# Performance work log

Hardware: AMD Instinct MI355X
Metric: run time of the kernel (lower is better)

The kernel has to match this reference:

```python
import jax, jax.numpy as jnp
import numpy as np

DMODEL = 1024

def setup_inputs() -> dict:
    key = jax.random.key(0)
    ks = jax.random.split(key, 7)
    scale = 1.0 / np.sqrt(DMODEL)
    x = jax.random.normal(ks[0], (4, 2048, DMODEL), dtype=jnp.float32)
    Wq = jax.random.normal(ks[1], (DMODEL, DMODEL), dtype=jnp.float32) * scale
    bq = jnp.zeros((DMODEL,), dtype=jnp.float32)
    Wk = jax.random.normal(ks[2], (DMODEL, DMODEL), dtype=jnp.float32) * scale
    bk = jnp.zeros((DMODEL,), dtype=jnp.float32)
    Wv = jax.random.normal(ks[3], (DMODEL, DMODEL), dtype=jnp.float32) * scale
    bv = jnp.zeros((DMODEL,), dtype=jnp.float32)
    return {"x": x, "Wq": Wq, "bq": bq, "Wk": Wk, "bk": bk, "Wv": Wv, "bv": bv}

def reference(x, Wq, bq, Wk, bk, Wv, bv):
    # QKV projections: [b, s, d]
    q = jnp.einsum('bsd,de->bse', x, Wq) + bq
    k = jnp.einsum('bsd,de->bse', x, Wk) + bk
    v = jnp.einsum('bsd,de->bse', x, Wv) + bv
    # scaled dot-product attention, full [b, s, s] score matrix (as in source)
    scores = jnp.einsum('bqd,bkd->bqk', q, k) / jnp.sqrt(jnp.asarray(q.shape[-1], q.dtype))
    weights = jax.nn.softmax(scores, axis=-1)
    return jnp.einsum('bqk,bkd->bqd', weights, v)
```

## Files before the change

kernel.cpp:

```cpp
#include <hip/hip_runtime.h>

typedef unsigned short u16;
typedef __attribute__((ext_vector_type(8))) short short8;
typedef __attribute__((ext_vector_type(4))) short short4v;
typedef __attribute__((ext_vector_type(4))) float f32x4;


__device__ __forceinline__ u16 f2bf(float f) {
  union { float f; unsigned u; } c; c.f = f;
  unsigned u = c.u;
  unsigned r = u + 0x7fffu + ((u >> 16) & 1u);
  return (u16)(r >> 16);
}

__device__ __forceinline__ float bf2f(u16 b) {
  union { unsigned u; float f; } c; c.u = ((unsigned)b) << 16;
  return c.f;
}

__device__ __forceinline__ void load_lds16(const void* g, void* l) {
  __builtin_amdgcn_global_load_lds(
      (__attribute__((address_space(1))) void*)(__UINTPTR_TYPE__)(g),
      (__attribute__((address_space(3))) void*)(l),
      16, 0, 0);
}

template <int N> __device__ __forceinline__ void vm_wait() {
  if constexpr (N == 0) asm volatile("s_waitcnt vmcnt(0)");
  else if constexpr (N == 3) asm volatile("s_waitcnt vmcnt(3)");
  else if constexpr (N == 4) asm volatile("s_waitcnt vmcnt(4)");
}

template <int BM, int MODE>
__global__ __launch_bounds__(512)
void gemm256(const u16* __restrict__ A, const u16* __restrict__ Bt,
             void* __restrict__ C0, void* __restrict__ C1,
             const float* __restrict__ b0, const float* __restrict__ b1,
             const float* __restrict__ b2,
             int K, int lda, int ldb, int ldc, float scale,
             long zsA, long zsB, long zsC)
{
  constexpr int MREP = BM / 32;
  constexpr int LA   = BM / 128;
  constexpr int BOFF = BM * 64;
  constexpr int LDSE = BM * 64 + 16384;
  __shared__ __align__(16) u16 lds[2][LDSE];

  A  += (long)blockIdx.z * zsA;
  Bt += (long)blockIdx.z * zsB;

  int bxi, byi;
  if (MODE == 0 || MODE == 3) {
    const int gw   = gridDim.x;
    const int nwg  = gw * gridDim.y;
    const int orig = blockIdx.x + gw * blockIdx.y;
    const int s    = (orig & 7) * (nwg >> 3) + (orig >> 3);
    bxi = s % gw; byi = s / gw;
  } else {
    bxi = blockIdx.x; byi = blockIdx.y;
  }

  const int t    = threadIdx.x;
  const int lane = t & 63;
  const int wave = t >> 6;
  const int wr   = wave >> 2;
  const int wc   = wave & 3;
  const long brow = (long)byi * BM;
  const long bcol = (long)bxi * 256;

  f32x4 acc[MREP][4];
#pragma unroll
  for (int m = 0; m < MREP; ++m)
#pragma unroll
    for (int n = 0; n < 4; ++n)
#pragma unroll
      for (int j = 0; j < 4; ++j) acc[m][n][j] = 0.f;

  const int frA  = wr * (BM / 2) + (lane & 15);
  const int kAsw = (((lane >> 4) ^ ((frA >> 1) & 3)) * 8);
  const int frB  = wc * 64 + (lane & 15);
  const int kBsw = (((lane >> 4) ^ ((frB >> 1) & 3)) * 8);

  const int sr  = t >> 2;
  const int ssl = ((t & 3) ^ ((sr >> 1) & 3)) * 8;
  const u16* gA = A  + (size_t)(brow + sr) * lda + ssl;
  const u16* gB = Bt + (size_t)(bcol + sr) * ldb + ssl;
  const int NT = K >> 6;

#define STAGE_A(nb, kt1, ks) do {                                   \
    u16* d = &lds[(nb)][(ks) * (BM * 32) + t * 8];                  \
    const u16* g = gA + (size_t)(kt1) * 64 + (ks) * 32;             \
    load_lds16(g, d);                                               \
    if (LA == 2) load_lds16(g + (size_t)128 * lda, d + 4096);       \
  } while (0)

#define STAGE_B(nb, kt1, ks) do {                                   \
    u16* d = &lds[(nb)][BOFF + (ks) * 8192 + t * 8];                \
    const u16* g = gB + (size_t)(kt1) * 64 + (ks) * 32;             \
    load_lds16(g, d);                                               \
    load_lds16(g + (size_t)128 * ldb, d + 4096);                    \
  } while (0)

#define PHASE2(ks, STG, VM) {                                                    \
    _Pragma("unroll")                                                            \
    for (int i = 0; i < MREP; ++i)                                               \
      af[i] = *(const short8*)&bufA[(ks) * (BM * 32) +                           \
                 (size_t)(frA + i * 16) * 32 + kAsw];                            \
    _Pragma("unroll")                                                            \
    for (int n = 0; n < 4; ++n)                                                  \
      bf[n] = *(const short8*)&bufB[(ks) * 8192 +                                \
                 (size_t)(frB + n * 16) * 32 + kBsw];                            \
    STG;                                                                         \
    __builtin_amdgcn_s_barrier();                                                \
    asm volatile("s_waitcnt lgkmcnt(0)");                                        \
    __builtin_amdgcn_sched_barrier(0);                                           \
    __builtin_amdgcn_s_setprio(1);                                               \
    _Pragma("unroll")                                                            \
    for (int i = 0; i < MREP; ++i)                                               \
      _Pragma("unroll")                                                          \
      for (int n = 0; n < 4; ++n)                                                \
        acc[i][n] = __builtin_amdgcn_mfma_f32_16x16x32_bf16(                     \
            af[i], bf[n], acc[i][n], 0, 0, 0);                                   \
    __builtin_amdgcn_s_setprio(0);                                               \
    VM;                                                                          \
    __builtin_amdgcn_s_barrier();                                                \
  }

  STAGE_A(0, 0, 0); STAGE_B(0, 0, 0); STAGE_A(0, 0, 1); STAGE_B(0, 0, 1);
  vm_wait<0>();
  __builtin_amdgcn_s_barrier();

  short8 af[MREP], bf[4];
  for (int kt = 0; kt < NT - 1; ++kt) {
    const u16* bufA = &lds[kt & 1][0];
    const u16* bufB = bufA + BOFF;
    const int nb = (kt + 1) & 1;
    PHASE2(0, { STAGE_A(nb, kt + 1, 0); STAGE_B(nb, kt + 1, 0); }, vm_wait<LA + 2>())
    PHASE2(1, { STAGE_A(nb, kt + 1, 1); STAGE_B(nb, kt + 1, 1); }, vm_wait<LA + 2>())
  }
  {
    const u16* bufA = &lds[(NT - 1) & 1][0];
    const u16* bufB = bufA + BOFF;
    PHASE2(0, (void)0, vm_wait<0>())
    PHASE2(1, (void)0, (void)0)
  }
#undef PHASE2
#undef STAGE_A
#undef STAGE_B

  const int dcol = lane & 15;
  const int dr4  = (lane >> 4) * 4;
  if (MODE == 0) {
    const int which = (int)(bcol >> 10);
    const float sc = which ? 1.0f : scale;
    const float* bb = which ? b1 : b0;
    u16* dst = (u16*)C0 + (long)which * (8192L * 1024);
#pragma unroll
    for (int m = 0; m < MREP; ++m) {
#pragma unroll
      for (int n = 0; n < 4; ++n) {
        const long cp   = (bcol - ((long)which << 10)) + wc * 64 + n * 16 + dcol;
        const long row0 = brow + wr * (BM / 2) + m * 16 + dr4;
        const float bias = bb[cp];
#pragma unroll
        for (int j = 0; j < 4; ++j)
          dst[(row0 + j) * 1024 + cp] = f2bf((acc[m][n][j] + bias) * sc);
      }
    }
  } else if (MODE == 3) {
    constexpr int SMSK = BM / 4 - 1;
    u16* sm = (u16*)lds;
#pragma unroll
    for (int m = 0; m < MREP; ++m) {
#pragma unroll
      for (int n = 0; n < 4; ++n) {
        const int cpl = wc * 64 + n * 16 + dcol;
        const int r0l = wr * (BM / 2) + m * 16 + dr4;
        const float bias = b2[bcol + cpl];
        short4v w;
#pragma unroll
        for (int j = 0; j < 4; ++j) w[j] = (short)f2bf(acc[m][n][j] + bias);
        *(short4v*)&sm[cpl * BM + (((r0l >> 2) ^ (cpl & SMSK)) << 2)] = w;
      }
    }
    __syncthreads();
    u16* dst = (u16*)C1;
#pragma unroll
    for (int it = 0; it < BM / 16; ++it) {
      const int idx = it * 512 + t;
      const int i  = idx / (BM / 8);
      const int ch = idx & (BM / 8 - 1);
      const short4v lo = *(const short4v*)&sm[i * BM + ((((ch * 2)    ) ^ (i & SMSK)) << 2)];
      const short4v hi = *(const short4v*)&sm[i * BM + ((((ch * 2) + 1) ^ (i & SMSK)) << 2)];
      short8 o;
      o[0] = lo[0]; o[1] = lo[1]; o[2] = lo[2]; o[3] = lo[3];
      o[4] = hi[0]; o[5] = hi[1]; o[6] = hi[2]; o[7] = hi[3];
      *(short8*)&dst[(bcol + i) * 8192 + brow + ch * 8] = o;
    }
  } else {
#pragma unroll
    for (int m = 0; m < MREP; ++m) {
#pragma unroll
      for (int n = 0; n < 4; ++n) {
        const long col  = bcol + wc * 64 + n * 16 + dcol;
        const long row0 = brow + wr * (BM / 2) + m * 16 + dr4;
        if (MODE == 1) {
#pragma unroll
          for (int j = 0; j < 4; ++j)
            ((u16*)C0)[(long)blockIdx.z * zsC + (row0 + j) * ldc + col] =
                f2bf(acc[m][n][j] * scale);
        } else {
#pragma unroll
          for (int j = 0; j < 4; ++j)
            ((float*)C0)[(long)blockIdx.z * zsC + (row0 + j) * ldc + col] =
                acc[m][n][j];
        }
      }
    }
  }
}

__global__ __launch_bounds__(256)
void cvt_bf16(const float* __restrict__ in, u16* __restrict__ out, int n4)
{
  int i = blockIdx.x * 256 + threadIdx.x;
  const int stride = gridDim.x * 256;
  for (; i < n4; i += stride) {
    const float4 f = ((const float4*)in)[i];
    ushort4 u;
    u.x = f2bf(f.x); u.y = f2bf(f.y); u.z = f2bf(f.z); u.w = f2bf(f.w);
    ((ushort4*)out)[i] = u;
  }
}

__global__ __launch_bounds__(256)
void wtrans(const float* __restrict__ W, u16* __restrict__ Wt)
{
  __shared__ u16 tile[32][33];
  const int tx = threadIdx.x;
  const int ty = threadIdx.y;
  const int bx = blockIdx.x * 32;
  const int by = blockIdx.y * 32;
#pragma unroll
  for (int i = 0; i < 4; ++i)
    tile[ty + i * 8][tx] = f2bf(W[(size_t)(by + ty + i * 8) * 1024 + bx + tx]);
  __syncthreads();
#pragma unroll
  for (int i = 0; i < 4; ++i)
    Wt[(size_t)(bx + ty + i * 8) * 1024 + by + tx] = tile[tx][ty + i * 8];
}

__global__ __launch_bounds__(256)
void softmax_rows_bf16(u16* __restrict__ S)
{
  u16* s = S + (size_t)blockIdx.x * 2048;
  const int t = threadIdx.x;

  const short8 r = ((const short8*)s)[t];
  float v[8];
#pragma unroll
  for (int i = 0; i < 8; ++i) v[i] = bf2f((u16)r[i]);

  float m = -1e30f;
#pragma unroll
  for (int i = 0; i < 8; ++i) m = fmaxf(m, v[i]);
#pragma unroll
  for (int o = 32; o; o >>= 1) m = fmaxf(m, __shfl_xor(m, o));
  __shared__ float redm[4], reds[4];
  if ((t & 63) == 0) redm[t >> 6] = m;
  __syncthreads();
  m = fmaxf(fmaxf(redm[0], redm[1]), fmaxf(redm[2], redm[3]));

  float sum = 0.f;
#pragma unroll
  for (int i = 0; i < 8; ++i) { v[i] = __expf(v[i] - m); sum += v[i]; }
#pragma unroll
  for (int o = 32; o; o >>= 1) sum += __shfl_xor(sum, o);
  if ((t & 63) == 0) reds[t >> 6] = sum;
  __syncthreads();
  const float inv = 1.f / (reds[0] + reds[1] + reds[2] + reds[3]);

  short8 w;
#pragma unroll
  for (int i = 0; i < 8; ++i) w[i] = (short)f2bf(v[i] * inv);
  ((short8*)s)[t] = w;
}

extern "C" void kernel_launch(void* const* d_in, const int* in_sizes, int n_in,
                              void* d_out, int out_size, void* d_ws, size_t ws_size,
                              hipStream_t stream)
{
  const float* x  = (const float*)d_in[0];
  const float* Wq = (const float*)d_in[1];
  const float* bq = (const float*)d_in[2];
  const float* Wk = (const float*)d_in[3];
  const float* bk = (const float*)d_in[4];
  const float* Wv = (const float*)d_in[5];
  const float* bv = (const float*)d_in[6];
  float* out = (float*)d_out;
  char* ws = (char*)d_ws;

  const size_t MB = (size_t)1 << 20;
  const float qscale = 0.03125f;
  const long  SO = 2048L * 1024;

  u16* Qb   = (u16*)(ws);
  u16* Kb   = (u16*)(ws + 16 * MB);
  u16* Vt   = (u16*)(ws + 32 * MB);
  u16* Sc   = (u16*)(ws + 48 * MB);
  u16* xb   = (u16*)(ws + 48 * MB);
  u16* Wcat = (u16*)(ws + 80 * MB);

  cvt_bf16<<<2048, 256, 0, stream>>>(x, xb, (4 * 2048 * 1024) / 4);
  dim3 tb(32, 8), tg(32, 32);
  wtrans<<<tg, tb, 0, stream>>>(Wq, Wcat);
  wtrans<<<tg, tb, 0, stream>>>(Wk, Wcat + 1024 * 1024);
  wtrans<<<tg, tb, 0, stream>>>(Wv, Wcat + 2 * 1024 * 1024);

  gemm256<256, 0><<<dim3(8, 32), 512, 0, stream>>>(
      xb, Wcat, Qb, nullptr, bq, bk, nullptr,
      1024, 1024, 1024, 1024, qscale, 0, 0, 0);

  gemm256<128, 3><<<dim3(4, 64), 512, 0, stream>>>(
      xb, Wcat + 2 * 1024 * 1024, nullptr, Vt, nullptr, nullptr, bv,
      1024, 1024, 1024, 1024, 1.0f, 0, 0, 0);

  gemm256<256, 1><<<dim3(8, 8, 4), 512, 0, stream>>>(
      Qb, Kb, Sc, nullptr, nullptr, nullptr, nullptr,
      1024, 1024, 1024, 2048, 1.0f, SO, SO, 2048L * 2048);

  softmax_rows_bf16<<<4 * 2048, 256, 0, stream>>>(Sc);

  gemm256<128, 2><<<dim3(4, 16, 4), 512, 0, stream>>>(
      Sc, Vt, out, nullptr, nullptr, nullptr, nullptr,
      2048, 2048, 8192, 1024, 1.0f, 2048L * 2048, 2048, SO);
}
```

Measured before the change: 175.7 us.

## Fuse softmax into the PV GEMM via a per-row log-sum-exp prologue

Removes the standalone row-softmax kernel. The PV GEMM gains a new mode with a prologue that computes each row's log-sum-exp over the full bf16 score row. It then exponentiates A fragments in registers (exp(s - L)) before each MFMA step. This saves a full read and write pass over the score matrix, but it recomputes exps redundantly in every column block and adds VALU work to the GEMM main loop. It also drops max-subtraction, so large scores could overflow. The block-index swizzle is also applied to every GEMM mode now, not just modes 0 and 3.

```diff
diff --git a/kernel.cpp b/kernel.cpp
--- a/kernel.cpp
+++ b/kernel.cpp
@@ -45,20 +45,18 @@
   constexpr int BOFF = BM * 64;
   constexpr int LDSE = BM * 64 + 16384;
   __shared__ __align__(16) u16 lds[2][LDSE];
+  __shared__ float Lrow[(MODE == 4) ? 128 : 1];
+  __shared__ float psum[(MODE == 4) ? 128 : 1][4];
 
   A  += (long)blockIdx.z * zsA;
   Bt += (long)blockIdx.z * zsB;
 
-  int bxi, byi;
-  if (MODE == 0 || MODE == 3) {
-    const int gw   = gridDim.x;
-    const int nwg  = gw * gridDim.y;
-    const int orig = blockIdx.x + gw * blockIdx.y;
-    const int s    = (orig & 7) * (nwg >> 3) + (orig >> 3);
-    bxi = s % gw; byi = s / gw;
-  } else {
-    bxi = blockIdx.x; byi = blockIdx.y;
-  }
+  const int gw   = gridDim.x;
+  const int nwg  = gw * gridDim.y;
+  const int orig = blockIdx.x + gw * blockIdx.y;
+  const int sswz = (orig & 7) * (nwg >> 3) + (orig >> 3);
+  const int bxi  = sswz % gw;
+  const int byi  = sswz / gw;
 
   const int t    = threadIdx.x;
   const int lane = t & 63;
@@ -80,6 +78,27 @@
   const int kAsw = (((lane >> 4) ^ ((frA >> 1) & 3)) * 8);
   const int frB  = wc * 64 + (lane & 15);
   const int kBsw = (((lane >> 4) ^ ((frB >> 1) & 3)) * 8);
+
+  float Lm[MREP];
+  if constexpr (MODE == 4) {
+    const int r = t >> 2;
+    const int q = t & 3;
+    const u16* p = A + (size_t)(brow + r) * lda + q * 8;
+    float ps = 0.f;
+#pragma unroll 8
+    for (int i = 0; i < 64; ++i) {
+      const short8 v = *(const short8*)(p + i * 32);
+#pragma unroll
+      for (int e = 0; e < 8; ++e) ps += __expf(bf2f((u16)v[e]));
+    }
+    psum[r][q] = ps;
+    __syncthreads();
+    if (t < 128)
+      Lrow[t] = __logf(psum[t][0] + psum[t][1] + psum[t][2] + psum[t][3]);
+    __syncthreads();
+#pragma unroll
+    for (int i = 0; i < MREP; ++i) Lm[i] = Lrow[frA + i * 16];
+  }
 
   const int sr  = t >> 2;
   const int ssl = ((t & 3) ^ ((sr >> 1) & 3)) * 8;
@@ -114,6 +133,16 @@
     __builtin_amdgcn_s_barrier();                                                \
     asm volatile("s_waitcnt lgkmcnt(0)");                                        \
     __builtin_amdgcn_sched_barrier(0);                                           \
+    if constexpr (MODE == 4) {                                                   \
+      _Pragma("unroll")                                                          \
+      for (int i = 0; i < MREP; ++i) {                                           \
+        short8 a = af[i];                                                        \
+        _Pragma("unroll")                                                        \
+        for (int e = 0; e < 8; ++e)                                              \
+          a[e] = (short)f2bf(__expf(bf2f((u16)a[e]) - Lm[i]));                   \
+        af[i] = a;                                                               \
+      }                                                                          \
+    }                                                                            \
     __builtin_amdgcn_s_setprio(1);                                               \
     _Pragma("unroll")                                                            \
     for (int i = 0; i < MREP; ++i)                                               \
@@ -248,42 +277,6 @@
 #pragma unroll
   for (int i = 0; i < 4; ++i)
     Wt[(size_t)(bx + ty + i * 8) * 1024 + by + tx] = tile[tx][ty + i * 8];
-}
-
-__global__ __launch_bounds__(256)
-void softmax_rows_bf16(u16* __restrict__ S)
-{
-  u16* s = S + (size_t)blockIdx.x * 2048;
-  const int t = threadIdx.x;
-
-  const short8 r = ((const short8*)s)[t];
-  float v[8];
-#pragma unroll
-  for (int i = 0; i < 8; ++i) v[i] = bf2f((u16)r[i]);
-
-  float m = -1e30f;
-#pragma unroll
-  for (int i = 0; i < 8; ++i) m = fmaxf(m, v[i]);
-#pragma unroll
-  for (int o = 32; o; o >>= 1) m = fmaxf(m, __shfl_xor(m, o));
-  __shared__ float redm[4], reds[4];
-  if ((t & 63) == 0) redm[t >> 6] = m;
-  __syncthreads();
-  m = fmaxf(fmaxf(redm[0], redm[1]), fmaxf(redm[2], redm[3]));
-
-  float sum = 0.f;
-#pragma unroll
-  for (int i = 0; i < 8; ++i) { v[i] = __expf(v[i] - m); sum += v[i]; }
-#pragma unroll
-  for (int o = 32; o; o >>= 1) sum += __shfl_xor(sum, o);
-  if ((t & 63) == 0) reds[t >> 6] = sum;
-  __syncthreads();
-  const float inv = 1.f / (reds[0] + reds[1] + reds[2] + reds[3]);
-
-  short8 w;
-#pragma unroll
-  for (int i = 0; i < 8; ++i) w[i] = (short)f2bf(v[i] * inv);
-  ((short8*)s)[t] = w;
 }
 
 extern "C" void kernel_launch(void* const* d_in, const int* in_sizes, int n_in,
@@ -329,9 +322,7 @@
       Qb, Kb, Sc, nullptr, nullptr, nullptr, nullptr,
       1024, 1024, 1024, 2048, 1.0f, SO, SO, 2048L * 2048);
 
-  softmax_rows_bf16<<<4 * 2048, 256, 0, stream>>>(Sc);
-
-  gemm256<128, 2><<<dim3(4, 16, 4), 512, 0, stream>>>(
+  gemm256<128, 4><<<dim3(4, 16, 4), 512, 0, stream>>>(
       Sc, Vt, out, nullptr, nullptr, nullptr, nullptr,
       2048, 2048, 8192, 1024, 1.0f, 2048L * 2048, 2048, SO);
 }
```

Measured after the change: 212.8 us. +21.1%, slower.
